# Performance work log

Hardware: AMD Instinct MI355X
Metric: run time of the kernel (lower is better)

The kernel has to match this reference:

```python
import jax, jax.numpy as jnp
import numpy as np

N_QUBITS = 16
BATCH = 512
NUM_CLASSES = 100


def _rx_mat(theta):
    """RX matrix; theta shape (...,) -> (..., 2, 2) complex64."""
    c = jnp.cos(theta / 2).astype(jnp.complex64)
    s = (-1j * jnp.sin(theta / 2)).astype(jnp.complex64)
    row0 = jnp.stack([c, s], axis=-1)
    row1 = jnp.stack([s, c], axis=-1)
    return jnp.stack([row0, row1], axis=-2)


def _rot_mat(phi, theta, omega):
    """qml.Rot = RZ(omega) RY(theta) RZ(phi); scalars/arrays -> (..., 2, 2)."""
    c = jnp.cos(theta / 2)
    s = jnp.sin(theta / 2)
    e_m = jnp.exp(-0.5j * (phi + omega).astype(jnp.complex64))
    e_p = jnp.exp(0.5j * (phi + omega).astype(jnp.complex64))
    e_dm = jnp.exp(-0.5j * (phi - omega).astype(jnp.complex64))
    e_dp = jnp.exp(0.5j * (phi - omega).astype(jnp.complex64))
    row0 = jnp.stack([e_m * c, -e_dp * s], axis=-1)
    row1 = jnp.stack([e_dm * s, e_p * c], axis=-1)
    return jnp.stack([row0, row1], axis=-2).astype(jnp.complex64)


def _apply_1q(state, U, w):
    """Apply shared (2,2) gate U on wire w. state: (B,) + (2,)*16."""
    s = jnp.moveaxis(state, w + 1, -1)
    s = jnp.einsum('ij,...j->...i', U, s)
    return jnp.moveaxis(s, -1, w + 1)


def _apply_1q_batched(state, U, w):
    """Apply per-sample (B,2,2) gate on wire w."""
    s = jnp.moveaxis(state, w + 1, -1)
    s = jnp.einsum('bij,b...j->b...i', U, s)
    return jnp.moveaxis(s, -1, w + 1)


def _apply_crx(state, theta, ctrl, tgt):
    """Controlled-RX(theta) with control ctrl, target tgt (shared scalar theta)."""
    U = _rx_mat(theta)
    s = jnp.moveaxis(state, (ctrl + 1, tgt + 1), (-2, -1))
    s1 = jnp.einsum('ij,...j->...i', U, s[..., 1, :])
    s = jnp.stack([s[..., 0, :], s1], axis=-2)
    return jnp.moveaxis(s, (-2, -1), (ctrl + 1, tgt + 1))


def _circuit(x, rot_l1, crx_l1, rot_l2, crx_l2):
    B = x.shape[0]
    # |0...0> initial state, shape (B, 2, 2, ..., 2)
    state = jnp.zeros((B,) + (2,) * N_QUBITS, dtype=jnp.complex64)
    state = state.at[(slice(None),) + (0,) * N_QUBITS].set(1.0)

    for layer_rot, layer_crx in ((rot_l1, crx_l1), (rot_l2, crx_l2)):
        # AngleEmbedding: RX(x[:, i]) on wire i (per-sample angles)
        for i in range(N_QUBITS):
            state = _apply_1q_batched(state, _rx_mat(x[:, i]), i)
        # Rot gates
        for i in range(N_QUBITS):
            U = _rot_mat(layer_rot[i, 0], layer_rot[i, 1], layer_rot[i, 2])
            state = _apply_1q(state, U, i)
        # ring CRX
        for i in range(N_QUBITS):
            state = _apply_crx(state, layer_crx[i, 0], i, (i + 1) % N_QUBITS)

    # <Z_i> = P(bit_i = 0) - P(bit_i = 1)
    probs = state.real ** 2 + state.imag ** 2  # (B,) + (2,)*16
    expvals = []
    for i in range(N_QUBITS):
        axes = tuple(a for a in range(1, N_QUBITS + 1) if a != i + 1)
        marg = probs.sum(axis=axes)  # (B, 2)
        expvals.append(marg[:, 0] - marg[:, 1])
    return jnp.stack(expvals, axis=1).astype(jnp.float32)  # (B, 16)


def setup_inputs() -> dict:
    key = jax.random.key(0)
    ks = jax.random.split(key, 7)
    return {
        'x': jax.random.normal(ks[0], (BATCH, N_QUBITS), jnp.float32),
        'rot_l1': jax.random.normal(ks[1], (N_QUBITS, 3), jnp.float32),
        'crx_l1': jax.random.normal(ks[2], (N_QUBITS, 1), jnp.float32),
        'rot_l2': jax.random.normal(ks[3], (N_QUBITS, 3), jnp.float32),
        'crx_l2': jax.random.normal(ks[4], (N_QUBITS, 1), jnp.float32),
        'W': jax.random.normal(ks[5], (NUM_CLASSES, N_QUBITS), jnp.float32) * 0.25,
        'b': jax.random.normal(ks[6], (NUM_CLASSES,), jnp.float32) * 0.01,
    }


def reference(x, rot_l1, crx_l1, rot_l2, crx_l2, W, b):
    feats = _circuit(x, rot_l1, crx_l1, rot_l2, crx_l2)  # (B, 16)
    logits = feats @ W.T + b  # (B, num_classes)
    return jax.nn.log_softmax(logits, axis=1)
```

## Files before the change

### kernel.cpp

```cpp
#include <hip/hip_runtime.h>
#include <math.h>

#define NQ 16
#define NBATCH 512
#define NCLS 100

typedef float v2f __attribute__((ext_vector_type(2)));
typedef __fp16 f16x2 __attribute__((ext_vector_type(2)));
typedef _Float16 half8 __attribute__((ext_vector_type(8)));
typedef float f32x4 __attribute__((ext_vector_type(4)));

__device__ __forceinline__ v2f mkv(float x, float y){ v2f r; r.x = x; r.y = y; return r; }
__device__ __forceinline__ f16x2 pack_h(v2f a){ return __builtin_amdgcn_cvt_pkrtz(a.x, a.y); }
__device__ __forceinline__ f16x2 pack_h2(float a, float b){ return __builtin_amdgcn_cvt_pkrtz(a, b); }
__device__ __forceinline__ v2f unpack_h(f16x2 h){ return mkv((float)h.x, (float)h.y); }

__device__ __forceinline__ unsigned pack_fp8(float a, float b){
  unsigned u;
  asm("v_cvt_pk_fp8_f32 %0, %1, %2" : "=v"(u) : "v"(a), "v"(b));
  return u;
}
__device__ __forceinline__ v2f unpack_fp8(unsigned u){
  v2f f;
  asm("v_cvt_pk_f32_fp8 %0, %1" : "=v"(f) : "v"(u));
  return f;
}

union pack16 { f16x2 h[4]; uint4 u; };

__device__ __forceinline__ v2f pk_cmul(v2f a, v2f b){
  v2f t, d;
  asm("v_pk_mul_f32 %0, %1, %2 op_sel:[0,0] op_sel_hi:[1,0]"
      : "=v"(t) : "v"(a), "v"(b));
  asm("v_pk_fma_f32 %0, %1, %2, %3 op_sel:[1,1,0] op_sel_hi:[0,1,1] neg_lo:[1,0,0]"
      : "=v"(d) : "v"(a), "v"(b), "v"(t));
  return d;
}
__device__ __forceinline__ v2f pk_cmul_acc(v2f a, v2f b, v2f acc){
  v2f t, d;
  asm("v_pk_fma_f32 %0, %1, %2, %3 op_sel:[0,0,0] op_sel_hi:[1,0,1]"
      : "=v"(t) : "v"(a), "v"(b), "v"(acc));
  asm("v_pk_fma_f32 %0, %1, %2, %3 op_sel:[1,1,0] op_sel_hi:[0,1,1] neg_lo:[1,0,0]"
      : "=v"(d) : "v"(a), "v"(b), "v"(t));
  return d;
}
__device__ __forceinline__ v2f pk_fma_el(v2f a, v2f b, v2f c){
  v2f d;
  asm("v_pk_fma_f32 %0, %1, %2, %3"
      : "=v"(d) : "v"(a), "v"(b), "v"(c));
  return d;
}
__device__ __forceinline__ void pk_rx(v2f &a, v2f &b, v2f cs){
  v2f t1, t2, na, nb;
  asm("v_pk_mul_f32 %0, %1, %2 op_sel:[0,0] op_sel_hi:[0,1]"
      : "=v"(t1) : "v"(cs), "v"(a));
  asm("v_pk_mul_f32 %0, %1, %2 op_sel:[0,0] op_sel_hi:[0,1]"
      : "=v"(t2) : "v"(cs), "v"(b));
  asm("v_pk_fma_f32 %0, %1, %2, %3 op_sel:[1,1,0] op_sel_hi:[1,0,1] neg_hi:[0,1,0]"
      : "=v"(na) : "v"(cs), "v"(b), "v"(t1));
  asm("v_pk_fma_f32 %0, %1, %2, %3 op_sel:[1,1,0] op_sel_hi:[1,0,1] neg_hi:[0,1,0]"
      : "=v"(nb) : "v"(cs), "v"(a), "v"(t2));
  a = na; b = nb;
}

template<int MT>
__device__ __forceinline__ void crx_pred(v2f (&v)[16], bool on, v2f cs){
  v2f id = mkv(1.f, 0.f);
  v2f cs_p = on ? cs : id;
  #pragma unroll
  for (int r=0;r<16;r++) if(!(r&MT)) pk_rx(v[r], v[r|MT], cs_p);
}
template<int MT>
__device__ __forceinline__ void crx_on(v2f (&v)[16], v2f cs){
  #pragma unroll
  for (int r=0;r<16;r++) if(!(r&MT)) pk_rx(v[r], v[r|MT], cs);
}
template<int MC,int MT>
__device__ __forceinline__ void crx_rr(v2f (&v)[16], v2f cs){
  #pragma unroll
  for (int r=0;r<16;r++) if((r&MC)&&!(r&MT)) pk_rx(v[r], v[r|MT], cs);
}
template<int M>
__device__ __forceinline__ void reg_gate(v2f (&v)[16], v2f u00, v2f u01, v2f u10, v2f u11){
  #pragma unroll
  for (int r=0;r<16;r++) if(!(r&M)){
    v2f a = v[r], b = v[r|M];
    v[r]   = pk_cmul_acc(u01, b, pk_cmul(u00, a));
    v[r|M] = pk_cmul_acc(u11, b, pk_cmul(u10, a));
  }
}
__device__ __forceinline__ void build_rxw(v2f cs, v2f w00, v2f w01, v2f w10, v2f w11,
      v2f &f00, v2f &f01, v2f &f10, v2f &f11){
  f00 = w00; f10 = w10; pk_rx(f00, f10, cs);
  f01 = w01; f11 = w11; pk_rx(f01, f11, cs);
}

__device__ __forceinline__ int lds_phys(int c){ return c ^ (((c>>4)^(c>>8))&15); }
__device__ __forceinline__ int swz(int m, int q){
  return m*4 + (q ^ (m&3) ^ ((m>>2)&3));
}
__device__ __forceinline__ int oswz(int idx){ return idx ^ ((idx>>5)&31); }

__global__ __launch_bounds__(256) void kprep(const float* __restrict__ x,
      const float* __restrict__ rot1, const float* __restrict__ crx1,
      const float* __restrict__ rot2, const float* __restrict__ crx2,
      v2f* __restrict__ fU, v2f* __restrict__ cm, float* __restrict__ expv)
{
  int t = blockIdx.x*blockDim.x + threadIdx.x;
  if (t < NBATCH*NQ) expv[t] = 0.f;
  if (t < 2*NBATCH*NQ){
    int w  = t & 15;
    int bb = (t>>4) & (NBATCH-1);
    int L  = t >> 13;
    const float* rot = L ? rot2 : rot1;
    float phi = rot[w*3+0], th = rot[w*3+1], om = rot[w*3+2];
    float ct = cosf(0.5f*th), stt = sinf(0.5f*th);
    float a1 = 0.5f*(phi+om), a2 = 0.5f*(phi-om);
    float emx = cosf(a1), emy = -sinf(a1);
    float epx = cosf(a1), epy =  sinf(a1);
    float edmx = cosf(a2), edmy = -sinf(a2);
    float edpx = cosf(a2), edpy =  sinf(a2);
    float R00x = emx*ct,   R00y = emy*ct;
    float R01x = -edpx*stt, R01y = -edpy*stt;
    float R10x = edmx*stt, R10y = edmy*stt;
    float R11x = epx*ct,   R11y = epy*ct;
    float xv = x[bb*NQ + w];
    float cx = cosf(0.5f*xv), sx = sinf(0.5f*xv);
    v2f* o = fU + (size_t)t*4;
    o[0] = mkv(R00x*cx + R01y*sx,  R00y*cx - R01x*sx);
    o[1] = mkv(R00y*sx + R01x*cx, -R00x*sx + R01y*cx);
    o[2] = mkv(R10x*cx + R11y*sx,  R10y*cx - R11x*sx);
    o[3] = mkv(R10y*sx + R11x*cx, -R10x*sx + R11y*cx);
  }
  if (t < 2*NQ){
    int L = t>>4, w = t&15;
    const float* cxl = L ? crx2 : crx1;
    float thc = cxl[w];
    cm[t] = mkv(cosf(0.5f*thc), sinf(0.5f*thc));
  }
}

__device__ __forceinline__ void store_Bfrag(_Float16* Bt16, size_t hb, int r0, const v2f (&v)[16]){
  int k0 = 2*r0;
  int lk = 16*(k0>>3);
  int j0 = k0 & 7;
  #pragma unroll
  for (int n=0;n<16;n++){
    _Float16 re  = (_Float16)v[n].x;
    _Float16 im  = (_Float16)v[n].y;
    _Float16 nim = (_Float16)(-v[n].y);
    size_t ln = (size_t)(lk + n);
    Bt16[((hb+0)*64 + ln)*8 + j0]   = re;
    Bt16[((hb+0)*64 + ln)*8 + j0+1] = nim;
    Bt16[((hb+1)*64 + ln)*8 + j0]   = im;
    Bt16[((hb+1)*64 + ln)*8 + j0+1] = re;
  }
}

__global__ __launch_bounds__(256) void kprepGall(const v2f* __restrict__ fU1,
      const v2f* __restrict__ fU2,
      const v2f* __restrict__ cm1, const v2f* __restrict__ cm2,
      _Float16* __restrict__ Bt16, _Float16* __restrict__ Bt16b,
      v2f* __restrict__ Tbl)
{
  int tt = blockIdx.x*blockDim.x + threadIdx.x;
  if (tt >= 2*32768 + 2*NBATCH) return;
  if (tt >= 2*32768){
    int t = tt - 2*32768;
    int bb = t >> 1, bit = t & 1;
    const v2f* U = fU1 + (size_t)bb*64;
    v2f p[16];
    p[0] = U[48]; p[1] = U[50];
    p[2] = pk_cmul(p[0], U[54]); p[3] = pk_cmul(p[1], U[54]);
    p[0] = pk_cmul(p[0], U[52]); p[1] = pk_cmul(p[1], U[52]);
    #pragma unroll
    for (int i=0;i<4;i++){ p[i+4]=pk_cmul(p[i],U[58]); p[i]=pk_cmul(p[i],U[56]); }
    #pragma unroll
    for (int i=0;i<8;i++){ p[i+8]=pk_cmul(p[i],U[62]); p[i]=pk_cmul(p[i],U[60]); }
    if (bit){
      #pragma unroll
      for (int r=0;r<16;r++) if(!(r&1)) pk_rx(p[r], p[r|1], cm1[11]);
    }
    #pragma unroll
    for (int r=0;r<16;r++) if((r&1)&&!(r&2)) pk_rx(p[r], p[r|2], cm1[12]);
    #pragma unroll
    for (int r=0;r<16;r++) if((r&2)&&!(r&4)) pk_rx(p[r], p[r|4], cm1[13]);
    #pragma unroll
    for (int r=0;r<16;r++) if((r&4)&&!(r&8)) pk_rx(p[r], p[r|8], cm1[14]);
    v2f* o = Tbl + ((size_t)bb<<5) + (bit<<4);
    #pragma unroll
    for (int r=0;r<16;r++) o[r] = p[r];
    return;
  }
  int which = tt >> 15;
  int t = tt & 32767;
  int r0 = t & 15;
  int var = (t>>4) & 1;
  int stage = (t>>5) & 1;
  int bg = t >> 6;
  const v2f* U2 = fU2 + ((size_t)bg<<6);
  v2f v[16];
  #pragma unroll
  for (int r=0;r<16;r++) v[r] = mkv(0.f,0.f);
  v[r0] = mkv(1.f,0.f);
  if (which == 0){
    if (stage == 0){
      reg_gate<1>(v, U2[28],U2[29],U2[30],U2[31]);
      reg_gate<2>(v, U2[32],U2[33],U2[34],U2[35]);
      reg_gate<4>(v, U2[36],U2[37],U2[38],U2[39]);
      reg_gate<8>(v, U2[40],U2[41],U2[42],U2[43]);
      if (var) crx_on<1>(v, cm2[6]);
      crx_rr<1,2>(v, cm2[7]);
      crx_rr<2,4>(v, cm2[8]);
      crx_rr<4,8>(v, cm2[9]);
    } else {
      reg_gate<1>(v, U2[44],U2[45],U2[46],U2[47]);
      reg_gate<2>(v, U2[48],U2[49],U2[50],U2[51]);
      reg_gate<4>(v, U2[52],U2[53],U2[54],U2[55]);
      reg_gate<8>(v, U2[56],U2[57],U2[58],U2[59]);
      if (var) crx_on<1>(v, cm2[10]);
      crx_rr<1,2>(v, cm2[11]);
      crx_rr<2,4>(v, cm2[12]);
      crx_rr<4,8>(v, cm2[13]);
    }
    size_t hb = (((size_t)bg*2 + stage)*2 + var)*2;
    store_Bfrag(Bt16, hb, r0, v);
  } else {
    if (stage == 0){
      if (var) crx_on<1>(v, cm1[15]);
      reg_gate<1>(v, U2[0], U2[1], U2[2], U2[3]);
      reg_gate<2>(v, U2[4], U2[5], U2[6], U2[7]);
      reg_gate<4>(v, U2[8], U2[9], U2[10],U2[11]);
      reg_gate<8>(v, U2[12],U2[13],U2[14],U2[15]);
      crx_rr<1,2>(v, cm2[0]);
      crx_rr<2,4>(v, cm2[1]);
      crx_rr<4,8>(v, cm2[2]);
    } else {
      reg_gate<1>(v, U2[16],U2[17],U2[18],U2[19]);
      reg_gate<2>(v, U2[20],U2[21],U2[22],U2[23]);
      reg_gate<4>(v, U2[24],U2[25],U2[26],U2[27]);
      if (var) crx_on<1>(v, cm2[3]);
      crx_rr<1,2>(v, cm2[4]);
      crx_rr<2,4>(v, cm2[5]);
    }
    size_t hb = (((size_t)bg*2 + stage)*2 + var)*2;
    store_Bfrag(Bt16b, hb, r0, v);
  }
}

__global__ __launch_bounds__(256) void kpass1(const v2f* __restrict__ fU1,
      const v2f* __restrict__ cm1, f16x2* __restrict__ compact)
{
  int lane = threadIdx.x & 63;
  int wv = threadIdx.x >> 6;
  int bg = blockIdx.x;
  const v2f* U = fU1 + ((size_t)bg<<6);
  v2f a = (lane&1) ? U[2] : U[0];
  a = pk_cmul(a, ((lane>>1)&1) ? U[22] : U[20]);
  a = pk_cmul(a, ((lane>>2)&1) ? U[26] : U[24]);
  a = pk_cmul(a, ((lane>>3)&1) ? U[30] : U[28]);
  a = pk_cmul(a, ((lane>>4)&1) ? U[34] : U[32]);
  a = pk_cmul(a, ((lane>>5)&1) ? U[38] : U[36]);
  a = pk_cmul(a, (wv&1) ? U[42] : U[40]);
  a = pk_cmul(a, ((wv>>1)&1) ? U[46] : U[44]);
  v2f v[16];
  v[0] = pk_cmul(a, U[4]);    v[1] = pk_cmul(a, U[6]);
  v[2] = pk_cmul(v[0], U[10]); v[3] = pk_cmul(v[1], U[10]);
  v[0] = pk_cmul(v[0], U[8]);  v[1] = pk_cmul(v[1], U[8]);
  #pragma unroll
  for (int i=0;i<4;i++){ v[i+4]=pk_cmul(v[i],U[14]); v[i]=pk_cmul(v[i],U[12]); }
  #pragma unroll
  for (int i=0;i<8;i++){ v[i+8]=pk_cmul(v[i],U[18]); v[i]=pk_cmul(v[i],U[16]); }
  crx_pred<1>(v, (lane&1)!=0, cm1[0]);
  crx_rr<1,2>(v, cm1[1]);
  crx_rr<2,4>(v, cm1[2]);
  crx_rr<4,8>(v, cm1[3]);
  __shared__ v2f lds[4096];
  #pragma unroll
  for (int r=0;r<16;r++){
    int c = (lane&1) | (r<<1) | (((lane>>1)&31)<<5) | (wv<<10);
    lds[lds_phys(c)] = v[r];
  }
  __syncthreads();
  #pragma unroll
  for (int r=0;r<16;r++){
    int c = ((lane>>1)&15) | ((lane&1)<<4) | (r<<5) | (((lane>>5)&1)<<9) | (wv<<10);
    v[r] = lds[lds_phys(c)];
  }
  crx_pred<1>(v, (lane&1)!=0, cm1[4]);
  crx_rr<1,2>(v, cm1[5]);
  crx_rr<2,4>(v, cm1[6]);
  crx_rr<4,8>(v, cm1[7]);
  __syncthreads();
  #pragma unroll
  for (int r=0;r<16;r++){
    int c = ((lane>>1)&15) | ((lane&1)<<4) | (r<<5) | (((lane>>5)&1)<<9) | (wv<<10);
    lds[lds_phys(c)] = v[r];
  }
  __syncthreads();
  #pragma unroll
  for (int r=0;r<16;r++){
    int c = (lane&63) | (wv<<6) | (((r>>3)&1)<<8) | ((r&7)<<9);
    v[r] = lds[lds_phys(c)];
  }
  crx_rr<8,1>(v, cm1[8]);
  crx_rr<1,2>(v, cm1[9]);
  crx_rr<2,4>(v, cm1[10]);
  __syncthreads();
  #pragma unroll
  for (int r=0;r<16;r++){
    int c = (lane&63) | (wv<<6) | (((r>>3)&1)<<8) | ((r&7)<<9);
    lds[lds_phys(c)] = v[r];
  }
  __syncthreads();
  f16x2* outp = compact + ((size_t)bg<<12);
  #pragma unroll
  for (int r=0;r<16;r++){
    int c = ((lane>>1)&31) | (wv<<5) | (r<<7) | ((lane&1)<<11);
    outp[lane | (wv<<6) | (r<<8)] = pack_h(lds[lds_phys(c)]);
  }
}

__global__ __launch_bounds__(256) void kpass2(const f16x2* __restrict__ compact,
      const v2f* __restrict__ Tbl, const half8* __restrict__ Btab2,
      unsigned short* __restrict__ st, int b0)
{
  int lane = threadIdx.x & 63;
  int wv = threadIdx.x >> 6;
  int blk = blockIdx.x;
  int bl = blk >> 4, h = blk & 15;
  int bg = b0 + bl;
  __shared__ uint4 lbuf[1024];
  f16x2* lbufH = (f16x2*)lbuf;

  v2f a = unpack_h(compact[((size_t)bg<<12) | (size_t)(lane | (wv<<6) | (h<<8))]);
  const v2f* T = Tbl + ((size_t)bg<<5) + ((lane&1)<<4);
  int sel = wv & 1;
  size_t hb1 = (((size_t)bg*2 + 0)*2 + sel)*2;
  size_t hb2 = (((size_t)bg*2 + 1)*2 + sel)*2;
  half8 B1a = Btab2[(hb1+0)*64 + lane];
  half8 B2a = Btab2[(hb1+1)*64 + lane];
  f32x4 zz = {0.f, 0.f, 0.f, 0.f};

  int kb = (lane>>1) & 15;
  int mA_fix = (lane&1) | ((lane>>5)<<4) | ((wv&1)<<5) | ((wv>>1)<<7);
  #pragma unroll
  for (int r=0;r<16;r++){
    v2f val = pk_cmul(a, T[r]);
    int m = mA_fix | ((r&7)<<1) | ((r>>3)<<6);
    lbufH[swz(m, kb>>2)*4 + (kb&3)] = pack_h(val);
  }
  __syncthreads();
  uint4 af1[4];
  #pragma unroll
  for (int t=0;t<4;t++){
    int m = (wv<<6) | (t<<4) | (lane&15);
    af1[t] = lbuf[swz(m, lane>>4)];
  }
  __syncthreads();

  f32x4 dre[4], dim[4];
  #pragma unroll
  for (int t=0;t<4;t++){
    half8 af = *(const half8*)&af1[t];
    dre[t] = __builtin_amdgcn_mfma_f32_16x16x32_f16(af, B1a, zz, 0, 0, 0);
    dim[t] = __builtin_amdgcn_mfma_f32_16x16x32_f16(af, B2a, zz, 0, 0, 0);
  }
  int n = lane & 15, lq = lane >> 4;
  int q_c = ((wv>>1)&1) | ((n&1)<<1);
  #pragma unroll
  for (int reg=0;reg<4;reg++){
    int mC = (lq&1) | (((n>>1)&1)<<1) | (((n>>2)&1)<<2) | ((lq>>1)<<3)
           | ((reg&1)<<4) | (((reg>>1)&1)<<5) | (((n>>3)&1)<<6) | ((wv&1)<<7);
    pack16 pk;
    #pragma unroll
    for (int t=0;t<4;t++) pk.h[t] = pack_h2(dre[t][reg], dim[t][reg]);
    lbuf[swz(mC, q_c)] = pk.u;
  }
  __syncthreads();
  uint4 af2[4];
  #pragma unroll
  for (int t2=0;t2<4;t2++){
    int m = (wv<<6) | (t2<<4) | (lane&15);
    af2[t2] = lbuf[swz(m, lane>>4)];
  }
  __syncthreads();

  half8 B1b = Btab2[(hb2+0)*64 + lane];
  half8 B2b = Btab2[(hb2+1)*64 + lane];
  #pragma unroll
  for (int t2=0;t2<4;t2++){
    half8 af = *(const half8*)&af2[t2];
    f32x4 ere = __builtin_amdgcn_mfma_f32_16x16x32_f16(af, B1b, zz, 0, 0, 0);
    f32x4 eim = __builtin_amdgcn_mfma_f32_16x16x32_f16(af, B2b, zz, 0, 0, 0);
    #pragma unroll
    for (int reg=0;reg<4;reg++){
      int idx = ((lane>>3)&1) | (((reg>>1)&1)<<1) | ((t2&1)<<2) | (((t2>>1)&1)<<3)
              | ((reg&1)<<4) | ((wv&1)<<5) | (((lane>>4)&1)<<6) | (((lane>>5)&1)<<7)
              | ((lane&1)<<8) | (((lane>>1)&1)<<9) | (((lane>>2)&1)<<10) | (((wv>>1)&1)<<11);
      lbufH[oswz(idx)] = pack_h2(ere[reg], eim[reg]);
    }
  }
  __syncthreads();

  unsigned short* S = st + ((size_t)bl<<16);
  #pragma unroll
  for (int r=0;r<16;r++){
    int idx = lane | (wv<<6) | (r<<8);
    f16x2 hv = lbufH[oswz(idx)];
    unsigned p8 = pack_fp8((float)hv.x, (float)hv.y);
    S[idx | (h<<12)] = (unsigned short)p8;
  }
}

__global__ __launch_bounds__(256) void kpass3(const unsigned short* __restrict__ st,
      const v2f* __restrict__ fU2, const v2f* __restrict__ cm2,
      const half8* __restrict__ Btab,
      float* __restrict__ expv, int b0)
{
  int lane = threadIdx.x & 63;
  int wv = threadIdx.x >> 6;
  int blk = blockIdx.x;
  int bl = blk >> 4, h = blk & 15;
  int bg = b0 + bl;
  const unsigned short* S = st + ((size_t)bl<<16);
  const v2f* U2 = fU2 + ((size_t)bg<<6);
  __shared__ uint4 lbuf[1024];

  int abase = (((h>>1)&1)<<5) | ((h&1)<<6) | (((h>>2)&1)<<8) | (((h>>3)&1)<<9)
            | ((wv&1)<<10) | (((wv>>1)&1)<<11);
  f16x2 v[16];
  #pragma unroll
  for (int r=0;r<16;r++){
    unsigned short u8 = S[(lane&31) | (((lane>>5)&1)<<7) | abase | (r<<12)];
    v2f fr = unpack_fp8((unsigned)u8);
    v[r] = pack_h(fr);
  }
  int m1 = ((lane>>2)&15) | (((wv>>1)&1)<<4) | ((lane&1)<<5)
         | ((wv&1)<<6) | (((lane>>1)&1)<<7);
  #pragma unroll
  for (int q=0;q<4;q++){
    pack16 pk;
    pk.h[0]=v[4*q]; pk.h[1]=v[4*q+1]; pk.h[2]=v[4*q+2]; pk.h[3]=v[4*q+3];
    lbuf[swz(m1,q)] = pk.u;
  }
  int sel = wv & 1;
  size_t hb1 = (((size_t)bg*2 + 0)*2 + sel)*2;
  size_t hb2 = (((size_t)bg*2 + 1)*2 + sel)*2;
  half8 B1a = Btab[(hb1+0)*64 + lane];
  half8 B2a = Btab[(hb1+1)*64 + lane];
  f32x4 zz = {0.f, 0.f, 0.f, 0.f};
  __syncthreads();
  uint4 af1[4];
  #pragma unroll
  for (int t=0;t<4;t++){
    int m = (wv<<6) | (t<<4) | (lane&15);
    af1[t] = lbuf[swz(m, lane>>4)];
  }
  __syncthreads();

  {
    int n = lane & 15;
    int q2 = lane >> 4;
    #pragma unroll
    for (int t=0;t<4;t++){
      half8 af = *(const half8*)&af1[t];
      f32x4 dre = __builtin_amdgcn_mfma_f32_16x16x32_f16(af, B1a, zz, 0, 0, 0);
      f32x4 dim = __builtin_amdgcn_mfma_f32_16x16x32_f16(af, B2a, zz, 0, 0, 0);
      int m2 = t | ((n&7)<<2) | (((wv>>1)&1)<<5) | (((n>>3)&1)<<6) | ((wv&1)<<7);
      pack16 pk;
      #pragma unroll
      for (int rg=0;rg<4;rg++) pk.h[rg] = pack_h2(dre[rg], dim[rg]);
      lbuf[swz(m2, q2)] = pk.u;
    }
  }
  __syncthreads();
  uint4 af2[4];
  #pragma unroll
  for (int t2=0;t2<4;t2++){
    int m = (wv<<6) | (t2<<4) | (lane&15);
    af2[t2] = lbuf[swz(m, lane>>4)];
  }

  half8 B1b = Btab[(hb2+0)*64 + lane];
  half8 B2b = Btab[(hb2+1)*64 + lane];
  v2f G00, G01, G10, G11;
  {
    v2f g00=U2[60], g01=U2[61], g10=U2[62], g11=U2[63];
    v2f f00,f01,f10,f11;
    build_rxw(cm2[14], g00,g01,g10,g11, f00,f01,f10,f11);
    bool on3 = ((lane>>3)&1) != 0;
    G00 = on3?f00:g00; G01 = on3?f01:g01; G10 = on3?f10:g10; G11 = on3?f11:g11;
  }
  v2f accT = mkv(0.f,0.f), acc15 = mkv(0.f,0.f), acc0 = mkv(0.f,0.f);
  v2f acc9 = mkv(0.f,0.f), acc1 = mkv(0.f,0.f);
  #pragma unroll
  for (int t2=0;t2<4;t2++){
    half8 af = *(const half8*)&af2[t2];
    f32x4 ere = __builtin_amdgcn_mfma_f32_16x16x32_f16(af, B1b, zz, 0, 0, 0);
    f32x4 eim = __builtin_amdgcn_mfma_f32_16x16x32_f16(af, B2b, zz, 0, 0, 0);
    v2f a0 = mkv(ere[0], eim[0]);
    v2f a1 = mkv(ere[1], eim[1]);
    v2f a2 = mkv(ere[2], eim[2]);
    v2f a3 = mkv(ere[3], eim[3]);
    v2f n0 = pk_cmul_acc(G01, a1, pk_cmul(G00, a0));
    v2f n1 = pk_cmul_acc(G11, a1, pk_cmul(G10, a0));
    v2f n2 = pk_cmul_acc(G01, a3, pk_cmul(G00, a2));
    v2f n3 = pk_cmul_acc(G11, a3, pk_cmul(G10, a2));
    pk_rx(n1, n3, cm2[15]);
    v2f q0 = pk_fma_el(n0,n0,mkv(0,0));
    v2f q1 = pk_fma_el(n1,n1,mkv(0,0));
    v2f q2v = pk_fma_el(n2,n2,mkv(0,0));
    v2f q3 = pk_fma_el(n3,n3,mkv(0,0));
    v2f qs = q0+q1+q2v+q3;
    accT += qs;
    acc15 += q1+q3;
    acc0  += q2v+q3;
    if (t2&1) acc9 += qs;
    if (t2&2) acc1 += qs;
  }
  float tot = accT.x + accT.y;
  float S15 = acc15.x + acc15.y;
  float S0w = acc0.x + acc0.y;
  float S9  = acc9.x + acc9.y;
  float S1w = acc1.x + acc1.y;
  float s = tot;
  float u[6];
  #pragma unroll
  for (int b=0;b<6;b++){
    int m = 1<<b;
    float tt = __shfl_xor(s, m, 64);
    u[b] = s - tt;
    s = s + tt;
    #pragma unroll
    for (int j=0;j<6;j++) if (j<b) u[j] += __shfl_xor(u[j], m, 64);
  }
  #pragma unroll
  for (int d=1; d<64; d<<=1){
    S15 += __shfl_xor(S15, d, 64);
    S0w += __shfl_xor(S0w, d, 64);
    S9  += __shfl_xor(S9, d, 64);
    S1w += __shfl_xor(S1w, d, 64);
  }
  __syncthreads();
  float* ef = (float*)lbuf;
  if (lane==0){
    ef[wv*16+11]=u[0]; ef[wv*16+12]=u[1]; ef[wv*16+13]=u[2]; ef[wv*16+14]=u[3];
    ef[wv*16+7]=u[4];  ef[wv*16+8]=u[5];
    ef[wv*16+15]=s-2.f*S15; ef[wv*16+0]=s-2.f*S0w;
    ef[wv*16+9]=s-2.f*S9;   ef[wv*16+1]=s-2.f*S1w;
    ef[wv*16+10]=(wv&1)?-s:s; ef[wv*16+6]=(wv&2)?-s:s;
    ef[wv*16+2]=(h&1)?-s:s; ef[wv*16+3]=(h&2)?-s:s;
    ef[wv*16+4]=(h&4)?-s:s; ef[wv*16+5]=(h&8)?-s:s;
  }
  __syncthreads();
  if (threadIdx.x < 16){
    float r4 = ef[threadIdx.x]+ef[16+threadIdx.x]+ef[32+threadIdx.x]+ef[48+threadIdx.x];
    atomicAdd(expv + (size_t)bg*NQ + threadIdx.x, r4);
  }
}

__global__ __launch_bounds__(128) void klogits(const float* __restrict__ expv,
      const float* __restrict__ W, const float* __restrict__ bias,
      float* __restrict__ out)
{
  int b = blockIdx.x;
  int tid = threadIdx.x;
  __shared__ float f[NQ];
  __shared__ float lg[128];
  __shared__ float red[128];
  if (tid < NQ) f[tid] = expv[b*NQ + tid];
  __syncthreads();
  float acc = -1e30f;
  if (tid < NCLS){
    acc = bias[tid];
    #pragma unroll
    for (int i=0;i<NQ;i++) acc += f[i]*W[tid*NQ+i];
  }
  lg[tid] = acc;
  red[tid] = acc;
  __syncthreads();
  #pragma unroll
  for (int sft=64; sft>0; sft>>=1){
    if (tid < sft) red[tid] = fmaxf(red[tid], red[tid+sft]);
    __syncthreads();
  }
  float m = red[0];
  __syncthreads();
  float e = (tid < NCLS) ? expf(lg[tid]-m) : 0.f;
  red[tid] = e;
  __syncthreads();
  #pragma unroll
  for (int sft=64; sft>0; sft>>=1){
    if (tid < sft) red[tid] = red[tid] + red[tid+sft];
    __syncthreads();
  }
  float lsum = logf(red[0]);
  if (tid < NCLS) out[b*NCLS+tid] = lg[tid] - m - lsum;
}

extern "C" void kernel_launch(void* const* d_in, const int* in_sizes, int n_in,
                              void* d_out, int out_size, void* d_ws, size_t ws_size,
                              hipStream_t stream)
{
  const float* x    = (const float*)d_in[0];
  const float* rot1 = (const float*)d_in[1];
  const float* crx1 = (const float*)d_in[2];
  const float* rot2 = (const float*)d_in[3];
  const float* crx2 = (const float*)d_in[4];
  const float* W    = (const float*)d_in[5];
  const float* bias = (const float*)d_in[6];
  float* out = (float*)d_out;

  char* ws = (char*)d_ws;
  float* expv = (float*)ws;
  v2f*   fU   = (v2f*)(ws + (40<<10));
  v2f*   cmm  = (v2f*)(ws + (560<<10));
  v2f*   Tbl  = (v2f*)(ws + (564<<10));
  _Float16* Bt16  = (_Float16*)(ws + (704<<10));
  _Float16* Bt16b = (_Float16*)(ws + (4800<<10));
  f16x2* compact = (f16x2*)(ws + (8896<<10));
  const size_t stOff = (size_t)(8896<<10) + ((size_t)NBATCH<<14);
  unsigned short* st = (unsigned short*)(ws + stOff);

  kprep<<<(2*NBATCH*NQ + 255)/256, 256, 0, stream>>>(x, rot1, crx1, rot2, crx2, fU, cmm, expv);

  v2f* fU1 = fU;
  v2f* fU2 = fU + 32768;
  v2f* cm1 = cmm;
  v2f* cm2 = cmm + 16;

  kprepGall<<<(2*32768 + 2*NBATCH + 255)/256, 256, 0, stream>>>(fU1, fU2, cm1, cm2, Bt16, Bt16b, Tbl);
  kpass1<<<NBATCH, 256, 0, stream>>>(fU1, cm1, compact);

  size_t avail = (ws_size > stOff) ? (ws_size - stOff) : 0;
  int chunk = NBATCH;
  while (chunk > 1 && (size_t)chunk*65536*sizeof(unsigned short) > avail) chunk >>= 1;

  for (int b0 = 0; b0 < NBATCH; b0 += chunk){
    kpass2<<<chunk*16, 256, 0, stream>>>(compact, Tbl, (const half8*)Bt16b, st, b0);
    kpass3<<<chunk*16, 256, 0, stream>>>(st, fU2, cm2, (const half8*)Bt16, expv, b0);
  }
  klogits<<<NBATCH, 128, 0, stream>>>(expv, W, bias, out);
}
```

Measured before the change: 97.40 us.

## Process two h-slices per block in pass2/pass3 and remap block indices

```diff
diff --git a/kernel.cpp b/kernel.cpp
--- a/kernel.cpp
+++ b/kernel.cpp
@@ -327,89 +327,92 @@
 {
   int lane = threadIdx.x & 63;
   int wv = threadIdx.x >> 6;
-  int blk = blockIdx.x;
-  int bl = blk >> 4, h = blk & 15;
+  int g = blockIdx.x;
+  int cx = g & 7, q = g >> 3;
+  int h8 = q & 7;
+  int bl = cx + 8*(q>>3);
   int bg = b0 + bl;
   __shared__ uint4 lbuf[1024];
   f16x2* lbufH = (f16x2*)lbuf;
 
-  v2f a = unpack_h(compact[((size_t)bg<<12) | (size_t)(lane | (wv<<6) | (h<<8))]);
   const v2f* T = Tbl + ((size_t)bg<<5) + ((lane&1)<<4);
   int sel = wv & 1;
   size_t hb1 = (((size_t)bg*2 + 0)*2 + sel)*2;
   size_t hb2 = (((size_t)bg*2 + 1)*2 + sel)*2;
   half8 B1a = Btab2[(hb1+0)*64 + lane];
   half8 B2a = Btab2[(hb1+1)*64 + lane];
+  half8 B1b = Btab2[(hb2+0)*64 + lane];
+  half8 B2b = Btab2[(hb2+1)*64 + lane];
   f32x4 zz = {0.f, 0.f, 0.f, 0.f};
-
   int kb = (lane>>1) & 15;
   int mA_fix = (lane&1) | ((lane>>5)<<4) | ((wv&1)<<5) | ((wv>>1)<<7);
-  #pragma unroll
-  for (int r=0;r<16;r++){
-    v2f val = pk_cmul(a, T[r]);
-    int m = mA_fix | ((r&7)<<1) | ((r>>3)<<6);
-    lbufH[swz(m, kb>>2)*4 + (kb&3)] = pack_h(val);
-  }
-  __syncthreads();
-  uint4 af1[4];
-  #pragma unroll
-  for (int t=0;t<4;t++){
-    int m = (wv<<6) | (t<<4) | (lane&15);
-    af1[t] = lbuf[swz(m, lane>>4)];
-  }
-  __syncthreads();
-
-  f32x4 dre[4], dim[4];
-  #pragma unroll
-  for (int t=0;t<4;t++){
-    half8 af = *(const half8*)&af1[t];
-    dre[t] = __builtin_amdgcn_mfma_f32_16x16x32_f16(af, B1a, zz, 0, 0, 0);
-    dim[t] = __builtin_amdgcn_mfma_f32_16x16x32_f16(af, B2a, zz, 0, 0, 0);
-  }
   int n = lane & 15, lq = lane >> 4;
   int q_c = ((wv>>1)&1) | ((n&1)<<1);
-  #pragma unroll
-  for (int reg=0;reg<4;reg++){
-    int mC = (lq&1) | (((n>>1)&1)<<1) | (((n>>2)&1)<<2) | ((lq>>1)<<3)
-           | ((reg&1)<<4) | (((reg>>1)&1)<<5) | (((n>>3)&1)<<6) | ((wv&1)<<7);
-    pack16 pk;
-    #pragma unroll
-    for (int t=0;t<4;t++) pk.h[t] = pack_h2(dre[t][reg], dim[t][reg]);
-    lbuf[swz(mC, q_c)] = pk.u;
-  }
-  __syncthreads();
-  uint4 af2[4];
-  #pragma unroll
-  for (int t2=0;t2<4;t2++){
-    int m = (wv<<6) | (t2<<4) | (lane&15);
-    af2[t2] = lbuf[swz(m, lane>>4)];
-  }
-  __syncthreads();
-
-  half8 B1b = Btab2[(hb2+0)*64 + lane];
-  half8 B2b = Btab2[(hb2+1)*64 + lane];
-  #pragma unroll
-  for (int t2=0;t2<4;t2++){
-    half8 af = *(const half8*)&af2[t2];
-    f32x4 ere = __builtin_amdgcn_mfma_f32_16x16x32_f16(af, B1b, zz, 0, 0, 0);
-    f32x4 eim = __builtin_amdgcn_mfma_f32_16x16x32_f16(af, B2b, zz, 0, 0, 0);
+  unsigned short* S = st + ((size_t)bl<<16);
+
+  for (int hh=0; hh<2; hh++){
+    int h = h8 + 8*hh;
+    if (hh) __syncthreads();
+    v2f a = unpack_h(compact[((size_t)bg<<12) | (size_t)(lane | (wv<<6) | (h<<8))]);
+    #pragma unroll
+    for (int r=0;r<16;r++){
+      v2f val = pk_cmul(a, T[r]);
+      int m = mA_fix | ((r&7)<<1) | ((r>>3)<<6);
+      lbufH[swz(m, kb>>2)*4 + (kb&3)] = pack_h(val);
+    }
+    __syncthreads();
+    uint4 af1[4];
+    #pragma unroll
+    for (int t=0;t<4;t++){
+      int m = (wv<<6) | (t<<4) | (lane&15);
+      af1[t] = lbuf[swz(m, lane>>4)];
+    }
+    __syncthreads();
+    f32x4 dre[4], dim[4];
+    #pragma unroll
+    for (int t=0;t<4;t++){
+      half8 af = *(const half8*)&af1[t];
+      dre[t] = __builtin_amdgcn_mfma_f32_16x16x32_f16(af, B1a, zz, 0, 0, 0);
+      dim[t] = __builtin_amdgcn_mfma_f32_16x16x32_f16(af, B2a, zz, 0, 0, 0);
+    }
     #pragma unroll
     for (int reg=0;reg<4;reg++){
-      int idx = ((lane>>3)&1) | (((reg>>1)&1)<<1) | ((t2&1)<<2) | (((t2>>1)&1)<<3)
-              | ((reg&1)<<4) | ((wv&1)<<5) | (((lane>>4)&1)<<6) | (((lane>>5)&1)<<7)
-              | ((lane&1)<<8) | (((lane>>1)&1)<<9) | (((lane>>2)&1)<<10) | (((wv>>1)&1)<<11);
-      lbufH[oswz(idx)] = pack_h2(ere[reg], eim[reg]);
-    }
-  }
-  __syncthreads();
-
-  unsigned short* S = st + ((size_t)bl<<16);
-  #pragma unroll
-  for (int r=0;r<16;r++){
-    int idx = lane | (wv<<6) | (r<<8);
-    f16x2 hv = lbufH[oswz(idx)];
-    unsigned p8 = pack_fp8((float)hv.x, (float)hv.y);
-    S[idx | (h<<12)] = (unsigned short)p8;
+      int mC = (lq&1) | (((n>>1)&1)<<1) | (((n>>2)&1)<<2) | ((lq>>1)<<3)
+             | ((reg&1)<<4) | (((reg>>1)&1)<<5) | (((n>>3)&1)<<6) | ((wv&1)<<7);
+      pack16 pk;
+      #pragma unroll
+      for (int t=0;t<4;t++) pk.h[t] = pack_h2(dre[t][reg], dim[t][reg]);
+      lbuf[swz(mC, q_c)] = pk.u;
+    }
+    __syncthreads();
+    uint4 af2[4];
+    #pragma unroll
+    for (int t2=0;t2<4;t2++){
+      int m = (wv<<6) | (t2<<4) | (lane&15);
+      af2[t2] = lbuf[swz(m, lane>>4)];
+    }
+    __syncthreads();
+    #pragma unroll
+    for (int t2=0;t2<4;t2++){
+      half8 af = *(const half8*)&af2[t2];
+      f32x4 ere = __builtin_amdgcn_mfma_f32_16x16x32_f16(af, B1b, zz, 0, 0, 0);
+      f32x4 eim = __builtin_amdgcn_mfma_f32_16x16x32_f16(af, B2b, zz, 0, 0, 0);
+      #pragma unroll
+      for (int reg=0;reg<4;reg++){
+        int idx = ((lane>>3)&1) | (((reg>>1)&1)<<1) | ((t2&1)<<2) | (((t2>>1)&1)<<3)
+                | ((reg&1)<<4) | ((wv&1)<<5) | (((lane>>4)&1)<<6) | (((lane>>5)&1)<<7)
+                | ((lane&1)<<8) | (((lane>>1)&1)<<9) | (((lane>>2)&1)<<10) | (((wv>>1)&1)<<11);
+        lbufH[oswz(idx)] = pack_h2(ere[reg], eim[reg]);
+      }
+    }
+    __syncthreads();
+    #pragma unroll
+    for (int r=0;r<16;r++){
+      int idx = lane | (wv<<6) | (r<<8);
+      f16x2 hv = lbufH[oswz(idx)];
+      unsigned p8 = pack_fp8((float)hv.x, (float)hv.y);
+      S[idx | (h<<12)] = (unsigned short)p8;
+    }
   }
 }
 
@@ -420,70 +423,23 @@
 {
   int lane = threadIdx.x & 63;
   int wv = threadIdx.x >> 6;
-  int blk = blockIdx.x;
-  int bl = blk >> 4, h = blk & 15;
+  int g = blockIdx.x;
+  int cx = g & 7, q = g >> 3;
+  int h8 = q & 7;
+  int bl = cx + 8*(q>>3);
   int bg = b0 + bl;
   const unsigned short* S = st + ((size_t)bl<<16);
   const v2f* U2 = fU2 + ((size_t)bg<<6);
   __shared__ uint4 lbuf[1024];
 
-  int abase = (((h>>1)&1)<<5) | ((h&1)<<6) | (((h>>2)&1)<<8) | (((h>>3)&1)<<9)
-            | ((wv&1)<<10) | (((wv>>1)&1)<<11);
-  f16x2 v[16];
-  #pragma unroll
-  for (int r=0;r<16;r++){
-    unsigned short u8 = S[(lane&31) | (((lane>>5)&1)<<7) | abase | (r<<12)];
-    v2f fr = unpack_fp8((unsigned)u8);
-    v[r] = pack_h(fr);
-  }
-  int m1 = ((lane>>2)&15) | (((wv>>1)&1)<<4) | ((lane&1)<<5)
-         | ((wv&1)<<6) | (((lane>>1)&1)<<7);
-  #pragma unroll
-  for (int q=0;q<4;q++){
-    pack16 pk;
-    pk.h[0]=v[4*q]; pk.h[1]=v[4*q+1]; pk.h[2]=v[4*q+2]; pk.h[3]=v[4*q+3];
-    lbuf[swz(m1,q)] = pk.u;
-  }
   int sel = wv & 1;
   size_t hb1 = (((size_t)bg*2 + 0)*2 + sel)*2;
   size_t hb2 = (((size_t)bg*2 + 1)*2 + sel)*2;
   half8 B1a = Btab[(hb1+0)*64 + lane];
   half8 B2a = Btab[(hb1+1)*64 + lane];
-  f32x4 zz = {0.f, 0.f, 0.f, 0.f};
-  __syncthreads();
-  uint4 af1[4];
-  #pragma unroll
-  for (int t=0;t<4;t++){
-    int m = (wv<<6) | (t<<4) | (lane&15);
-    af1[t] = lbuf[swz(m, lane>>4)];
-  }
-  __syncthreads();
-
-  {
-    int n = lane & 15;
-    int q2 = lane >> 4;
-    #pragma unroll
-    for (int t=0;t<4;t++){
-      half8 af = *(const half8*)&af1[t];
-      f32x4 dre = __builtin_amdgcn_mfma_f32_16x16x32_f16(af, B1a, zz, 0, 0, 0);
-      f32x4 dim = __builtin_amdgcn_mfma_f32_16x16x32_f16(af, B2a, zz, 0, 0, 0);
-      int m2 = t | ((n&7)<<2) | (((wv>>1)&1)<<5) | (((n>>3)&1)<<6) | ((wv&1)<<7);
-      pack16 pk;
-      #pragma unroll
-      for (int rg=0;rg<4;rg++) pk.h[rg] = pack_h2(dre[rg], dim[rg]);
-      lbuf[swz(m2, q2)] = pk.u;
-    }
-  }
-  __syncthreads();
-  uint4 af2[4];
-  #pragma unroll
-  for (int t2=0;t2<4;t2++){
-    int m = (wv<<6) | (t2<<4) | (lane&15);
-    af2[t2] = lbuf[swz(m, lane>>4)];
-  }
-
   half8 B1b = Btab[(hb2+0)*64 + lane];
   half8 B2b = Btab[(hb2+1)*64 + lane];
+  f32x4 zz = {0.f, 0.f, 0.f, 0.f};
   v2f G00, G01, G10, G11;
   {
     v2f g00=U2[60], g01=U2[61], g10=U2[62], g11=U2[63];
@@ -492,39 +448,99 @@
     bool on3 = ((lane>>3)&1) != 0;
     G00 = on3?f00:g00; G01 = on3?f01:g01; G10 = on3?f10:g10; G11 = on3?f11:g11;
   }
-  v2f accT = mkv(0.f,0.f), acc15 = mkv(0.f,0.f), acc0 = mkv(0.f,0.f);
+  int m1 = ((lane>>2)&15) | (((wv>>1)&1)<<4) | ((lane&1)<<5)
+         | ((wv&1)<<6) | (((lane>>1)&1)<<7);
+
+  v2f accT0 = mkv(0.f,0.f), accT1 = mkv(0.f,0.f);
+  v2f acc15 = mkv(0.f,0.f), acc0 = mkv(0.f,0.f);
   v2f acc9 = mkv(0.f,0.f), acc1 = mkv(0.f,0.f);
-  #pragma unroll
-  for (int t2=0;t2<4;t2++){
-    half8 af = *(const half8*)&af2[t2];
-    f32x4 ere = __builtin_amdgcn_mfma_f32_16x16x32_f16(af, B1b, zz, 0, 0, 0);
-    f32x4 eim = __builtin_amdgcn_mfma_f32_16x16x32_f16(af, B2b, zz, 0, 0, 0);
-    v2f a0 = mkv(ere[0], eim[0]);
-    v2f a1 = mkv(ere[1], eim[1]);
-    v2f a2 = mkv(ere[2], eim[2]);
-    v2f a3 = mkv(ere[3], eim[3]);
-    v2f n0 = pk_cmul_acc(G01, a1, pk_cmul(G00, a0));
-    v2f n1 = pk_cmul_acc(G11, a1, pk_cmul(G10, a0));
-    v2f n2 = pk_cmul_acc(G01, a3, pk_cmul(G00, a2));
-    v2f n3 = pk_cmul_acc(G11, a3, pk_cmul(G10, a2));
-    pk_rx(n1, n3, cm2[15]);
-    v2f q0 = pk_fma_el(n0,n0,mkv(0,0));
-    v2f q1 = pk_fma_el(n1,n1,mkv(0,0));
-    v2f q2v = pk_fma_el(n2,n2,mkv(0,0));
-    v2f q3 = pk_fma_el(n3,n3,mkv(0,0));
-    v2f qs = q0+q1+q2v+q3;
-    accT += qs;
-    acc15 += q1+q3;
-    acc0  += q2v+q3;
-    if (t2&1) acc9 += qs;
-    if (t2&2) acc1 += qs;
-  }
-  float tot = accT.x + accT.y;
+
+  for (int hh=0; hh<2; hh++){
+    int h = h8 + 8*hh;
+    if (hh) __syncthreads();
+    int abase = (((h>>1)&1)<<5) | ((h&1)<<6) | (((h>>2)&1)<<8) | (((h>>3)&1)<<9)
+              | ((wv&1)<<10) | (((wv>>1)&1)<<11);
+    f16x2 v[16];
+    #pragma unroll
+    for (int r=0;r<16;r++){
+      unsigned short u8 = S[(lane&31) | (((lane>>5)&1)<<7) | abase | (r<<12)];
+      v2f fr = unpack_fp8((unsigned)u8);
+      v[r] = pack_h(fr);
+    }
+    #pragma unroll
+    for (int qd=0;qd<4;qd++){
+      pack16 pk;
+      pk.h[0]=v[4*qd]; pk.h[1]=v[4*qd+1]; pk.h[2]=v[4*qd+2]; pk.h[3]=v[4*qd+3];
+      lbuf[swz(m1,qd)] = pk.u;
+    }
+    __syncthreads();
+    uint4 af1[4];
+    #pragma unroll
+    for (int t=0;t<4;t++){
+      int m = (wv<<6) | (t<<4) | (lane&15);
+      af1[t] = lbuf[swz(m, lane>>4)];
+    }
+    __syncthreads();
+    {
+      int n = lane & 15;
+      int q2 = lane >> 4;
+      #pragma unroll
+      for (int t=0;t<4;t++){
+        half8 af = *(const half8*)&af1[t];
+        f32x4 dre = __builtin_amdgcn_mfma_f32_16x16x32_f16(af, B1a, zz, 0, 0, 0);
+        f32x4 dim = __builtin_amdgcn_mfma_f32_16x16x32_f16(af, B2a, zz, 0, 0, 0);
+        int m2 = t | ((n&7)<<2) | (((wv>>1)&1)<<5) | (((n>>3)&1)<<6) | ((wv&1)<<7);
+        pack16 pk;
+        #pragma unroll
+        for (int rg=0;rg<4;rg++) pk.h[rg] = pack_h2(dre[rg], dim[rg]);
+        lbuf[swz(m2, q2)] = pk.u;
+      }
+    }
+    __syncthreads();
+    uint4 af2[4];
+    #pragma unroll
+    for (int t2=0;t2<4;t2++){
+      int m = (wv<<6) | (t2<<4) | (lane&15);
+      af2[t2] = lbuf[swz(m, lane>>4)];
+    }
+    v2f lT = mkv(0.f,0.f);
+    #pragma unroll
+    for (int t2=0;t2<4;t2++){
+      half8 af = *(const half8*)&af2[t2];
+      f32x4 ere = __builtin_amdgcn_mfma_f32_16x16x32_f16(af, B1b, zz, 0, 0, 0);
+      f32x4 eim = __builtin_amdgcn_mfma_f32_16x16x32_f16(af, B2b, zz, 0, 0, 0);
+      v2f a0 = mkv(ere[0], eim[0]);
+      v2f a1 = mkv(ere[1], eim[1]);
+      v2f a2 = mkv(ere[2], eim[2]);
+      v2f a3 = mkv(ere[3], eim[3]);
+      v2f n0 = pk_cmul_acc(G01, a1, pk_cmul(G00, a0));
+      v2f n1 = pk_cmul_acc(G11, a1, pk_cmul(G10, a0));
+      v2f n2 = pk_cmul_acc(G01, a3, pk_cmul(G00, a2));
+      v2f n3 = pk_cmul_acc(G11, a3, pk_cmul(G10, a2));
+      pk_rx(n1, n3, cm2[15]);
+      v2f q0 = pk_fma_el(n0,n0,mkv(0,0));
+      v2f q1 = pk_fma_el(n1,n1,mkv(0,0));
+      v2f q2v = pk_fma_el(n2,n2,mkv(0,0));
+      v2f q3 = pk_fma_el(n3,n3,mkv(0,0));
+      v2f qs = q0+q1+q2v+q3;
+      lT += qs;
+      acc15 += q1+q3;
+      acc0  += q2v+q3;
+      if (t2&1) acc9 += qs;
+      if (t2&2) acc1 += qs;
+    }
+    accT0 = (hh==0) ? (accT0+lT) : accT0;
+    accT1 = (hh==1) ? (accT1+lT) : accT1;
+  }
+
+  float tot0 = accT0.x + accT0.y;
+  float tot1 = accT1.x + accT1.y;
+  float s  = tot0 + tot1;
+  float dd = tot0 - tot1;
   float S15 = acc15.x + acc15.y;
   float S0w = acc0.x + acc0.y;
   float S9  = acc9.x + acc9.y;
   float S1w = acc1.x + acc1.y;
-  float s = tot;
   float u[6];
   #pragma unroll
   for (int b=0;b<6;b++){
@@ -536,11 +552,12 @@
     for (int j=0;j<6;j++) if (j<b) u[j] += __shfl_xor(u[j], m, 64);
   }
   #pragma unroll
-  for (int d=1; d<64; d<<=1){
-    S15 += __shfl_xor(S15, d, 64);
-    S0w += __shfl_xor(S0w, d, 64);
-    S9  += __shfl_xor(S9, d, 64);
-    S1w += __shfl_xor(S1w, d, 64);
+  for (int d1=1; d1<64; d1<<=1){
+    dd  += __shfl_xor(dd, d1, 64);
+    S15 += __shfl_xor(S15, d1, 64);
+    S0w += __shfl_xor(S0w, d1, 64);
+    S9  += __shfl_xor(S9, d1, 64);
+    S1w += __shfl_xor(S1w, d1, 64);
   }
   __syncthreads();
   float* ef = (float*)lbuf;
@@ -550,8 +567,8 @@
     ef[wv*16+15]=s-2.f*S15; ef[wv*16+0]=s-2.f*S0w;
     ef[wv*16+9]=s-2.f*S9;   ef[wv*16+1]=s-2.f*S1w;
     ef[wv*16+10]=(wv&1)?-s:s; ef[wv*16+6]=(wv&2)?-s:s;
-    ef[wv*16+2]=(h&1)?-s:s; ef[wv*16+3]=(h&2)?-s:s;
-    ef[wv*16+4]=(h&4)?-s:s; ef[wv*16+5]=(h&8)?-s:s;
+    ef[wv*16+2]=(h8&1)?-s:s; ef[wv*16+3]=(h8&2)?-s:s;
+    ef[wv*16+4]=(h8&4)?-s:s; ef[wv*16+5]=dd;
   }
   __syncthreads();
   if (threadIdx.x < 16){
@@ -635,11 +652,11 @@
 
   size_t avail = (ws_size > stOff) ? (ws_size - stOff) : 0;
   int chunk = NBATCH;
-  while (chunk > 1 && (size_t)chunk*65536*sizeof(unsigned short) > avail) chunk >>= 1;
+  while (chunk > 8 && (size_t)chunk*65536*sizeof(unsigned short) > avail) chunk >>= 1;
 
   for (int b0 = 0; b0 < NBATCH; b0 += chunk){
-    kpass2<<<chunk*16, 256, 0, stream>>>(compact, Tbl, (const half8*)Bt16b, st, b0);
-    kpass3<<<chunk*16, 256, 0, stream>>>(st, fU2, cm2, (const half8*)Bt16, expv, b0);
+    kpass2<<<chunk*8, 256, 0, stream>>>(compact, Tbl, (const half8*)Bt16b, st, b0);
+    kpass3<<<chunk*8, 256, 0, stream>>>(st, fU2, cm2, (const half8*)Bt16, expv, b0);
   }
   klogits<<<NBATCH, 128, 0, stream>>>(expv, W, bias, out);
 }
```

Measured after the change: 98.82 us. About the same (+1.5%).
